# Kernel tuning notes

Hardware: AMD Instinct MI355X
Metric: run time of the kernel (lower is better)

Reference implementation:

```python
import jax, jax.numpy as jnp
import numpy as np

B, T, D, E, P = 4, 2048, 1024, 8, 1024

def setup_inputs() -> dict:
    key = jax.random.key(0)
    k1, k2, k3 = jax.random.split(key, 3)
    x = jax.random.normal(k1, (B, T, D), dtype=jnp.float32)
    gate_w = jax.random.normal(k2, (D, E), dtype=jnp.float32) * (1.0 / np.sqrt(D))
    gate_b = jnp.zeros((E,), dtype=jnp.float32)
    expert_w = jax.random.normal(k3, (E, D, P), dtype=jnp.float32) * (1.0 / np.sqrt(D))
    expert_b = jnp.zeros((E, P), dtype=jnp.float32)
    return {"x": x, "gate_w": gate_w, "gate_b": gate_b,
            "expert_w": expert_w, "expert_b": expert_b}

def reference(x, gate_w, gate_b, expert_w, expert_b):
    # gating: Dense(E) with softmax -> [B, T, E]
    gate = jax.nn.softmax(jnp.einsum('btd,de->bte', x, gate_w) + gate_b, axis=-1)
    # all experts as one batched GEMM: [B, T, E, P]
    expert_out = jnp.einsum('btd,edp->btep', x, expert_w) + expert_b
    # gate-weighted sum over experts -> [B, T, P]
    out = jnp.einsum('bte,btep->btp', gate, expert_out)
    return out
```

## Files before the change

kernel.cpp:

```cpp
#include <hip/hip_runtime.h>
#include <hip/hip_bf16.h>
#include <math.h>

#define M_TOT 8192
#define D_DIM 1024
#define E_NUM 8
#define P_DIM 1024
#define K_TOT (E_NUM * D_DIM)

typedef __attribute__((ext_vector_type(8))) short short8;
typedef __attribute__((ext_vector_type(4))) float f32x4;
typedef __attribute__((ext_vector_type(8))) unsigned short u16x8;

static __device__ __forceinline__ unsigned short f2bf(float f) {
  unsigned u = __builtin_bit_cast(unsigned, f);
  unsigned r = (u + 0x7fffu + ((u >> 16) & 1u)) >> 16;
  return (unsigned short)r;
}

__global__ __launch_bounds__(256) void prep_m_kernel(const float* __restrict__ x,
                                                     const float* __restrict__ gw,
                                                     const float* __restrict__ gb,
                                                     const float* __restrict__ eb,
                                                     float* __restrict__ gate,
                                                     unsigned short* __restrict__ xb,
                                                     float* __restrict__ out) {
  __shared__ __align__(16) unsigned short lx[4][1024];
  const int wv   = threadIdx.x >> 6;
  const int lane = threadIdx.x & 63;
  const int row  = blockIdx.x * 4 + wv;
  const float* xr = x + (size_t)row * D_DIM;

  float acc[E_NUM];
#pragma unroll
  for (int e = 0; e < E_NUM; ++e) acc[e] = 0.f;
#pragma unroll
  for (int it = 0; it < 16; ++it) {
    const int d = it * 64 + lane;
    const float xv = xr[d];
    lx[wv][d] = f2bf(xv);
    const float4* g4 = reinterpret_cast<const float4*>(gw + (size_t)d * E_NUM);
    const float4 a = g4[0], b = g4[1];
    acc[0] += xv * a.x; acc[1] += xv * a.y; acc[2] += xv * a.z; acc[3] += xv * a.w;
    acc[4] += xv * b.x; acc[5] += xv * b.y; acc[6] += xv * b.z; acc[7] += xv * b.w;
  }
#pragma unroll
  for (int off = 32; off >= 1; off >>= 1) {
#pragma unroll
    for (int e = 0; e < E_NUM; ++e) acc[e] += __shfl_xor(acc[e], off, 64);
  }
  __syncthreads();

  float g[E_NUM], mx = -1e30f;
#pragma unroll
  for (int e = 0; e < E_NUM; ++e) { g[e] = acc[e] + gb[e]; mx = fmaxf(mx, g[e]); }
  float s = 0.f;
#pragma unroll
  for (int e = 0; e < E_NUM; ++e) { g[e] = expf(g[e] - mx); s += g[e]; }
  const float inv = 1.f / s;
#pragma unroll
  for (int e = 0; e < E_NUM; ++e) g[e] *= inv;
  if (lane == 0) {
#pragma unroll
    for (int e = 0; e < E_NUM; ++e) gate[(size_t)row * E_NUM + e] = g[e];
  }

  unsigned short* xrow = xb + (size_t)row * D_DIM;
#pragma unroll
  for (int h = 0; h < 2; ++h) {
    const int jd = lane * 2 + h;
    const int cbase = (jd >> 3) * 8 + ((jd & 7) ^ (row & 7));
    const u16x8 vv = *reinterpret_cast<const u16x8*>(&lx[wv][jd * 8]);
    *reinterpret_cast<u16x8*>(&xrow[cbase * 8]) = vv;
  }

  float* orow = out + (size_t)row * P_DIM;
#pragma unroll
  for (int q = 0; q < 4; ++q) {
    const int p = q * 256 + lane * 4;
    float4 sv = {0.f, 0.f, 0.f, 0.f};
#pragma unroll
    for (int e = 0; e < E_NUM; ++e) {
      const float4 b4 = *reinterpret_cast<const float4*>(&eb[(size_t)e * P_DIM + p]);
      sv.x += g[e] * b4.x; sv.y += g[e] * b4.y; sv.z += g[e] * b4.z; sv.w += g[e] * b4.w;
    }
    *reinterpret_cast<float4*>(&orow[p]) = sv;
  }
}

__global__ __launch_bounds__(256) void wtrans2_kernel(const float* __restrict__ w,
                                                      unsigned short* __restrict__ wt) {
  __shared__ float tile[64][65];
  const int e  = blockIdx.z;
  const int p0 = blockIdx.y * 64;
  const int d0 = blockIdx.x * 64;
  const int tx = threadIdx.x & 63;
  const int ty = threadIdx.x >> 6;
  const float* src = w + ((size_t)e * D_DIM + d0) * P_DIM + p0;
#pragma unroll
  for (int i = 0; i < 16; ++i) {
    const int dr = i * 4 + ty;
    tile[dr][tx] = src[(size_t)dr * P_DIM + tx];
  }
  __syncthreads();
#pragma unroll
  for (int i = 0; i < 16; ++i) {
    const int pr = i * 4 + ty;
    const int c = tx ^ ((pr & 7) << 3);
    wt[(size_t)(p0 + pr) * K_TOT + e * D_DIM + d0 + c] = f2bf(tile[tx][pr]);
  }
}

__global__ __launch_bounds__(256, 3) void gemm_ex2_kernel(
    const unsigned short* __restrict__ xb,
    const unsigned short* __restrict__ wt,
    const float* __restrict__ gate,
    float* __restrict__ out) {
  __shared__ unsigned short lA[128 * 64];
  __shared__ unsigned short lB[128 * 64];
  __shared__ float lG[128 * 8];

  const int tid  = threadIdx.x;
  const int lane = tid & 63;
  const int wid  = tid >> 6;
  const int wr   = wid >> 1, wc = wid & 1;

  const int bid = blockIdx.x;
  const int nt  = bid & 7;
  const int idx = bid >> 3;
  const int kh  = idx & 1;
  const int mt  = idx >> 1;
  const int m0  = mt * 128, n0 = nt * 128;

  reinterpret_cast<float4*>(lG)[tid] =
      reinterpret_cast<const float4*>(gate + (size_t)m0 * E_NUM)[tid];

  f32x4 acc[4][4];
#pragma unroll
  for (int i = 0; i < 4; ++i)
#pragma unroll
    for (int j = 0; j < 4; ++j)
#pragma unroll
      for (int k = 0; k < 4; ++k) acc[i][j][k] = 0.f;

  const int r0 = tid >> 3;
  const int c8 = tid & 7;
  const unsigned short* pAb = xb + (size_t)(m0 + r0) * D_DIM + c8 * 8;
  const unsigned short* pBb = wt + (size_t)(n0 + r0) * K_TOT + c8 * 8;

  for (int e = 0; e < 4; ++e) {
    const int eg = kh * 4 + e;
    if (e > 0) {
#pragma unroll
      for (int m = 0; m < 4; ++m) {
#pragma unroll
        for (int reg = 0; reg < 4; ++reg) {
          const int r = wr * 64 + m * 16 + (lane >> 4) * 4 + reg;
          const float ratio = lG[r * 8 + (eg - 1)] / lG[r * 8 + eg];
#pragma unroll
          for (int n = 0; n < 4; ++n) acc[m][n][reg] *= ratio;
        }
      }
    }
    const unsigned short* pB = pBb + (size_t)eg * D_DIM;
    for (int kt = 0; kt < 16; ++kt) {
      __syncthreads();
#pragma unroll
      for (int i = 0; i < 4; ++i) {
        __builtin_amdgcn_global_load_lds(
            (const __attribute__((address_space(1))) void*)(pAb + (size_t)i * 32 * D_DIM + kt * 64),
            (__attribute__((address_space(3))) void*)&lA[(tid + i * 256) * 8], 16, 0, 0);
      }
#pragma unroll
      for (int i = 0; i < 4; ++i) {
        __builtin_amdgcn_global_load_lds(
            (const __attribute__((address_space(1))) void*)(pB + (size_t)i * 32 * K_TOT + kt * 64),
            (__attribute__((address_space(3))) void*)&lB[(tid + i * 256) * 8], 16, 0, 0);
      }
      __syncthreads();
#pragma unroll
      for (int kk = 0; kk < 2; ++kk) {
        const int e0 = kk * 32 + (lane >> 4) * 8;
        short8 a[4], b[4];
#pragma unroll
        for (int m = 0; m < 4; ++m) {
          const int r = wr * 64 + m * 16 + (lane & 15);
          a[m] = *reinterpret_cast<const short8*>(&lA[r * 64 + (e0 ^ ((r & 7) << 3))]);
        }
#pragma unroll
        for (int n = 0; n < 4; ++n) {
          const int r = wc * 64 + n * 16 + (lane & 15);
          b[n] = *reinterpret_cast<const short8*>(&lB[r * 64 + (e0 ^ ((r & 7) << 3))]);
        }
#pragma unroll
        for (int m = 0; m < 4; ++m)
#pragma unroll
          for (int n = 0; n < 4; ++n)
            acc[m][n] = __builtin_amdgcn_mfma_f32_16x16x32_bf16(a[m], b[n], acc[m][n], 0, 0, 0);
      }
    }
  }

#pragma unroll
  for (int n = 0; n < 4; ++n) {
    const int cl = wc * 64 + n * 16 + (lane & 15);
#pragma unroll
    for (int m = 0; m < 4; ++m) {
#pragma unroll
      for (int reg = 0; reg < 4; ++reg) {
        const int r  = wr * 64 + m * 16 + (lane >> 4) * 4 + reg;
        const float gl = lG[r * 8 + kh * 4 + 3];
        atomicAdd(&out[(size_t)(m0 + r) * P_DIM + n0 + cl], acc[m][n][reg] * gl);
      }
    }
  }
}


__global__ __launch_bounds__(256) void gate_kernel(const float* __restrict__ x,
                                                   const float* __restrict__ gw,
                                                   const float* __restrict__ gb,
                                                   float* __restrict__ gate) {
  const int row  = blockIdx.x * 4 + (threadIdx.x >> 6);
  const int lane = threadIdx.x & 63;
  const float* xr = x + (size_t)row * D_DIM;
  float acc[E_NUM];
#pragma unroll
  for (int e = 0; e < E_NUM; ++e) acc[e] = 0.f;
#pragma unroll
  for (int it = 0; it < 16; ++it) {
    const int d = it * 64 + lane;
    const float xv = xr[d];
    const float4* g4 = reinterpret_cast<const float4*>(gw + (size_t)d * E_NUM);
    float4 a = g4[0], b = g4[1];
    acc[0] += xv * a.x; acc[1] += xv * a.y; acc[2] += xv * a.z; acc[3] += xv * a.w;
    acc[4] += xv * b.x; acc[5] += xv * b.y; acc[6] += xv * b.z; acc[7] += xv * b.w;
  }
#pragma unroll
  for (int off = 32; off >= 1; off >>= 1) {
#pragma unroll
    for (int e = 0; e < E_NUM; ++e) acc[e] += __shfl_xor(acc[e], off, 64);
  }
  if (lane == 0) {
    float v[E_NUM], mx = -1e30f;
#pragma unroll
    for (int e = 0; e < E_NUM; ++e) { v[e] = acc[e] + gb[e]; mx = fmaxf(mx, v[e]); }
    float s = 0.f;
#pragma unroll
    for (int e = 0; e < E_NUM; ++e) { v[e] = expf(v[e] - mx); s += v[e]; }
    const float inv = 1.f / s;
#pragma unroll
    for (int e = 0; e < E_NUM; ++e) gate[(size_t)row * E_NUM + e] = v[e] * inv;
  }
}

__global__ __launch_bounds__(256) void wtrans_kernel(const float* __restrict__ w,
                                                     unsigned short* __restrict__ wt) {
  __shared__ float tile[64][65];
  const int e  = blockIdx.z;
  const int p0 = blockIdx.y * 64;
  const int d0 = blockIdx.x * 64;
  const int tx = threadIdx.x & 63;
  const int ty = threadIdx.x >> 6;
  const float* src = w + ((size_t)e * D_DIM + d0) * P_DIM + p0;
#pragma unroll
  for (int i = 0; i < 16; ++i) {
    const int dr = i * 4 + ty;
    tile[dr][tx] = src[(size_t)dr * P_DIM + tx];
  }
  __syncthreads();
  unsigned short* dst = wt + ((size_t)e * P_DIM + p0) * D_DIM + d0;
#pragma unroll
  for (int i = 0; i < 16; ++i) {
    const int pr = i * 4 + ty;
    const int cc = tx ^ ((pr & 7) << 3);
    dst[(size_t)pr * D_DIM + cc] = f2bf(tile[tx][pr]);
  }
}

__global__ __launch_bounds__(256, 2) void moe_gemm_kernel(
    const float* __restrict__ x,
    const unsigned short* __restrict__ wt,
    const float* __restrict__ gate,
    const float* __restrict__ eb,
    float* __restrict__ out) {
  __shared__ unsigned short lA[128 * 64];
  __shared__ unsigned short lB[128 * 64];
  __shared__ float lG[128 * 8];
  __shared__ float lBias[E_NUM * 128];

  const int tid  = threadIdx.x;
  const int lane = tid & 63;
  const int wid  = tid >> 6;
  const int wr   = wid >> 1, wc = wid & 1;
  const int m0   = blockIdx.x * 128;
  const int n0   = blockIdx.y * 128;

  reinterpret_cast<float4*>(lG)[tid] =
      reinterpret_cast<const float4*>(gate + (size_t)m0 * E_NUM)[tid];
  {
    const int e = tid >> 5, cc = (tid & 31) * 4;
    *reinterpret_cast<float4*>(&lBias[e * 128 + cc]) =
        *reinterpret_cast<const float4*>(&eb[(size_t)e * P_DIM + n0 + cc]);
  }
  __syncthreads();

  const int rA   = tid >> 1;
  const int colA = (tid & 1) * 32;
  const float* xrow = x + (size_t)(m0 + rA) * D_DIM + colA;

  f32x4 acc[4][4];
#pragma unroll
  for (int i = 0; i < 4; ++i)
#pragma unroll
    for (int jj = 0; jj < 4; ++jj)
#pragma unroll
      for (int k = 0; k < 4; ++k) acc[i][jj][k] = 0.f;

  for (int e = 0; e < E_NUM; ++e) {
    const float gs = lG[rA * 8 + e];
    const unsigned short* wte = wt + ((size_t)e * P_DIM + n0) * D_DIM;
    for (int kt = 0; kt < 16; ++kt) {
      __syncthreads();
      const float4* apv = reinterpret_cast<const float4*>(xrow + kt * 64);
#pragma unroll
      for (int jj = 0; jj < 4; ++jj) {
        float4 p = apv[2 * jj], q = apv[2 * jj + 1];
        u16x8 v;
        v[0] = f2bf(p.x * gs); v[1] = f2bf(p.y * gs);
        v[2] = f2bf(p.z * gs); v[3] = f2bf(p.w * gs);
        v[4] = f2bf(q.x * gs); v[5] = f2bf(q.y * gs);
        v[6] = f2bf(q.z * gs); v[7] = f2bf(q.w * gs);
        const int idxw = rA * 64 + ((colA + jj * 8) ^ ((rA & 7) << 3));
        *reinterpret_cast<u16x8*>(&lA[idxw]) = v;
      }
#pragma unroll
      for (int i = 0; i < 4; ++i) {
        const int u  = tid + i * 256;
        const int rr = u >> 3;
        const int cc = u & 7;
        const unsigned short* src = wte + (size_t)rr * D_DIM + kt * 64 + cc * 8;
        __builtin_amdgcn_global_load_lds(
            (const __attribute__((address_space(1))) void*)src,
            (__attribute__((address_space(3))) void*)&lB[u * 8], 16, 0, 0);
      }
      __syncthreads();
#pragma unroll
      for (int kk = 0; kk < 2; ++kk) {
        const int e0 = kk * 32 + (lane >> 4) * 8;
        short8 a[4], b[4];
#pragma unroll
        for (int m = 0; m < 4; ++m) {
          const int r = wr * 64 + m * 16 + (lane & 15);
          a[m] = *reinterpret_cast<const short8*>(&lA[r * 64 + (e0 ^ ((r & 7) << 3))]);
        }
#pragma unroll
        for (int n = 0; n < 4; ++n) {
          const int r = wc * 64 + n * 16 + (lane & 15);
          b[n] = *reinterpret_cast<const short8*>(&lB[r * 64 + (e0 ^ ((r & 7) << 3))]);
        }
#pragma unroll
        for (int m = 0; m < 4; ++m)
#pragma unroll
          for (int n = 0; n < 4; ++n)
            acc[m][n] = __builtin_amdgcn_mfma_f32_16x16x32_bf16(a[m], b[n], acc[m][n], 0, 0, 0);
      }
    }
  }

#pragma unroll
  for (int m = 0; m < 4; ++m) {
#pragma unroll
    for (int n = 0; n < 4; ++n) {
      const int rbase = wr * 64 + m * 16 + ((lane >> 4) * 4);
      const int cl    = wc * 64 + n * 16 + (lane & 15);
#pragma unroll
      for (int reg = 0; reg < 4; ++reg) {
        const int r = rbase + reg;
        float bsum = 0.f;
#pragma unroll
        for (int e = 0; e < E_NUM; ++e) bsum += lG[r * 8 + e] * lBias[e * 128 + cl];
        out[(size_t)(m0 + r) * P_DIM + n0 + cl] = acc[m][n][reg] + bsum;
      }
    }
  }
}


extern "C" void kernel_launch(void* const* d_in, const int* in_sizes, int n_in,
                              void* d_out, int out_size, void* d_ws, size_t ws_size,
                              hipStream_t stream) {
  const float* x  = (const float*)d_in[0];
  const float* gw = (const float*)d_in[1];
  const float* gb = (const float*)d_in[2];
  const float* ew = (const float*)d_in[3];
  const float* eb = (const float*)d_in[4];
  float* out = (float*)d_out;

  char* ws = (char*)d_ws;
  float* gate        = (float*)ws;
  unsigned short* wt = (unsigned short*)(ws + 262144);

  const size_t need_new = 262144ull + 16777216ull + 16777216ull;

  if (ws_size >= need_new) {
    unsigned short* xbb = (unsigned short*)(ws + 262144 + 16777216);
    wtrans2_kernel<<<dim3(D_DIM / 64, P_DIM / 64, E_NUM), 256, 0, stream>>>(ew, wt);
    prep_m_kernel<<<M_TOT / 4, 256, 0, stream>>>(x, gw, gb, eb, gate, xbb, out);
    gemm_ex2_kernel<<<1024, 256, 0, stream>>>(xbb, wt, gate, out);
  } else {
    gate_kernel<<<M_TOT / 4, 256, 0, stream>>>(x, gw, gb, gate);
    wtrans_kernel<<<dim3(D_DIM / 64, P_DIM / 64, E_NUM), 256, 0, stream>>>(ew, wt);
    moe_gemm_kernel<<<dim3(M_TOT / 128, P_DIM / 128), 256, 0, stream>>>(x, wt, gate, eb, out);
  }
}
```

Before: 193.2 us.

## Fuse weight transpose and activation prep into one launch with vectorized stores

Merges the expert-weight transpose/bf16 conversion kernel and the gating/activation-prep kernel into a single launch, with block index ranges selecting which job a block does. This removes one kernel launch and lets the two independent prep phases run at the same time on the GPU. The transpose path now packs eight bf16 values per thread into one 16-byte store instead of scalar 2-byte stores, keeping the same swizzled layout at 8-element-chunk granularity. The combined kernel allocates both shared-memory arrays in every block, which may lower occupancy.

```diff
diff --git a/kernel.cpp b/kernel.cpp
--- a/kernel.cpp
+++ b/kernel.cpp
@@ -18,96 +18,104 @@
   return (unsigned short)r;
 }
 
-__global__ __launch_bounds__(256) void prep_m_kernel(const float* __restrict__ x,
-                                                     const float* __restrict__ gw,
-                                                     const float* __restrict__ gb,
-                                                     const float* __restrict__ eb,
-                                                     float* __restrict__ gate,
-                                                     unsigned short* __restrict__ xb,
-                                                     float* __restrict__ out) {
+__global__ __launch_bounds__(256) void prep_all_kernel(const float* __restrict__ x,
+                                                       const float* __restrict__ gw,
+                                                       const float* __restrict__ gb,
+                                                       const float* __restrict__ ew,
+                                                       const float* __restrict__ eb,
+                                                       float* __restrict__ gate,
+                                                       unsigned short* __restrict__ xb,
+                                                       unsigned short* __restrict__ wt,
+                                                       float* __restrict__ out) {
   __shared__ __align__(16) unsigned short lx[4][1024];
-  const int wv   = threadIdx.x >> 6;
-  const int lane = threadIdx.x & 63;
-  const int row  = blockIdx.x * 4 + wv;
-  const float* xr = x + (size_t)row * D_DIM;
-
-  float acc[E_NUM];
-#pragma unroll
-  for (int e = 0; e < E_NUM; ++e) acc[e] = 0.f;
-#pragma unroll
-  for (int it = 0; it < 16; ++it) {
-    const int d = it * 64 + lane;
-    const float xv = xr[d];
-    lx[wv][d] = f2bf(xv);
-    const float4* g4 = reinterpret_cast<const float4*>(gw + (size_t)d * E_NUM);
-    const float4 a = g4[0], b = g4[1];
-    acc[0] += xv * a.x; acc[1] += xv * a.y; acc[2] += xv * a.z; acc[3] += xv * a.w;
-    acc[4] += xv * b.x; acc[5] += xv * b.y; acc[6] += xv * b.z; acc[7] += xv * b.w;
-  }
-#pragma unroll
-  for (int off = 32; off >= 1; off >>= 1) {
-#pragma unroll
-    for (int e = 0; e < E_NUM; ++e) acc[e] += __shfl_xor(acc[e], off, 64);
-  }
-  __syncthreads();
-
-  float g[E_NUM], mx = -1e30f;
-#pragma unroll
-  for (int e = 0; e < E_NUM; ++e) { g[e] = acc[e] + gb[e]; mx = fmaxf(mx, g[e]); }
-  float s = 0.f;
-#pragma unroll
-  for (int e = 0; e < E_NUM; ++e) { g[e] = expf(g[e] - mx); s += g[e]; }
-  const float inv = 1.f / s;
-#pragma unroll
-  for (int e = 0; e < E_NUM; ++e) g[e] *= inv;
-  if (lane == 0) {
-#pragma unroll
-    for (int e = 0; e < E_NUM; ++e) gate[(size_t)row * E_NUM + e] = g[e];
-  }
-
-  unsigned short* xrow = xb + (size_t)row * D_DIM;
-#pragma unroll
-  for (int h = 0; h < 2; ++h) {
-    const int jd = lane * 2 + h;
-    const int cbase = (jd >> 3) * 8 + ((jd & 7) ^ (row & 7));
-    const u16x8 vv = *reinterpret_cast<const u16x8*>(&lx[wv][jd * 8]);
-    *reinterpret_cast<u16x8*>(&xrow[cbase * 8]) = vv;
-  }
-
-  float* orow = out + (size_t)row * P_DIM;
-#pragma unroll
-  for (int q = 0; q < 4; ++q) {
-    const int p = q * 256 + lane * 4;
-    float4 sv = {0.f, 0.f, 0.f, 0.f};
-#pragma unroll
-    for (int e = 0; e < E_NUM; ++e) {
-      const float4 b4 = *reinterpret_cast<const float4*>(&eb[(size_t)e * P_DIM + p]);
-      sv.x += g[e] * b4.x; sv.y += g[e] * b4.y; sv.z += g[e] * b4.z; sv.w += g[e] * b4.w;
-    }
-    *reinterpret_cast<float4*>(&orow[p]) = sv;
-  }
-}
-
-__global__ __launch_bounds__(256) void wtrans2_kernel(const float* __restrict__ w,
-                                                      unsigned short* __restrict__ wt) {
   __shared__ float tile[64][65];
-  const int e  = blockIdx.z;
-  const int p0 = blockIdx.y * 64;
-  const int d0 = blockIdx.x * 64;
-  const int tx = threadIdx.x & 63;
-  const int ty = threadIdx.x >> 6;
-  const float* src = w + ((size_t)e * D_DIM + d0) * P_DIM + p0;
-#pragma unroll
-  for (int i = 0; i < 16; ++i) {
-    const int dr = i * 4 + ty;
-    tile[dr][tx] = src[(size_t)dr * P_DIM + tx];
-  }
-  __syncthreads();
-#pragma unroll
-  for (int i = 0; i < 16; ++i) {
-    const int pr = i * 4 + ty;
-    const int c = tx ^ ((pr & 7) << 3);
-    wt[(size_t)(p0 + pr) * K_TOT + e * D_DIM + d0 + c] = f2bf(tile[tx][pr]);
+
+  if (blockIdx.x < 2048) {
+    const int wv   = threadIdx.x >> 6;
+    const int lane = threadIdx.x & 63;
+    const int row  = blockIdx.x * 4 + wv;
+    const float* xr = x + (size_t)row * D_DIM;
+
+    float acc[E_NUM];
+#pragma unroll
+    for (int e = 0; e < E_NUM; ++e) acc[e] = 0.f;
+#pragma unroll
+    for (int it = 0; it < 16; ++it) {
+      const int d = it * 64 + lane;
+      const float xv = xr[d];
+      lx[wv][d] = f2bf(xv);
+      const float4* g4 = reinterpret_cast<const float4*>(gw + (size_t)d * E_NUM);
+      const float4 a = g4[0], b = g4[1];
+      acc[0] += xv * a.x; acc[1] += xv * a.y; acc[2] += xv * a.z; acc[3] += xv * a.w;
+      acc[4] += xv * b.x; acc[5] += xv * b.y; acc[6] += xv * b.z; acc[7] += xv * b.w;
+    }
+#pragma unroll
+    for (int off = 32; off >= 1; off >>= 1) {
+#pragma unroll
+      for (int e = 0; e < E_NUM; ++e) acc[e] += __shfl_xor(acc[e], off, 64);
+    }
+    __syncthreads();
+
+    float g[E_NUM], mx = -1e30f;
+#pragma unroll
+    for (int e = 0; e < E_NUM; ++e) { g[e] = acc[e] + gb[e]; mx = fmaxf(mx, g[e]); }
+    float s = 0.f;
+#pragma unroll
+    for (int e = 0; e < E_NUM; ++e) { g[e] = expf(g[e] - mx); s += g[e]; }
+    const float inv = 1.f / s;
+#pragma unroll
+    for (int e = 0; e < E_NUM; ++e) g[e] *= inv;
+    if (lane == 0) {
+#pragma unroll
+      for (int e = 0; e < E_NUM; ++e) gate[(size_t)row * E_NUM + e] = g[e];
+    }
+
+    unsigned short* xrow = xb + (size_t)row * D_DIM;
+#pragma unroll
+    for (int h = 0; h < 2; ++h) {
+      const int jd = lane * 2 + h;
+      const int cbase = (jd >> 3) * 8 + ((jd & 7) ^ (row & 7));
+      const u16x8 vv = *reinterpret_cast<const u16x8*>(&lx[wv][jd * 8]);
+      *reinterpret_cast<u16x8*>(&xrow[cbase * 8]) = vv;
+    }
+
+    float* orow = out + (size_t)row * P_DIM;
+#pragma unroll
+    for (int q = 0; q < 4; ++q) {
+      const int p = q * 256 + lane * 4;
+      float4 sv = {0.f, 0.f, 0.f, 0.f};
+#pragma unroll
+      for (int e = 0; e < E_NUM; ++e) {
+        const float4 b4 = *reinterpret_cast<const float4*>(&eb[(size_t)e * P_DIM + p]);
+        sv.x += g[e] * b4.x; sv.y += g[e] * b4.y; sv.z += g[e] * b4.z; sv.w += g[e] * b4.w;
+      }
+      *reinterpret_cast<float4*>(&orow[p]) = sv;
+    }
+  } else {
+    const int bid2 = blockIdx.x - 2048;
+    const int e  = bid2 >> 8;
+    const int p0 = ((bid2 >> 4) & 15) * 64;
+    const int d0 = (bid2 & 15) * 64;
+    const int tx = threadIdx.x & 63;
+    const int ty = threadIdx.x >> 6;
+    const float* src = ew + ((size_t)e * D_DIM + d0) * P_DIM + p0;
+#pragma unroll
+    for (int i = 0; i < 16; ++i) {
+      const int dr = i * 4 + ty;
+      tile[dr][tx] = src[(size_t)dr * P_DIM + tx];
+    }
+    __syncthreads();
+#pragma unroll
+    for (int h = 0; h < 2; ++h) {
+      const int u  = threadIdx.x + h * 256;
+      const int pr = u >> 3;
+      const int ch = u & 7;
+      u16x8 v;
+#pragma unroll
+      for (int j = 0; j < 8; ++j) v[j] = f2bf(tile[ch * 8 + j][pr]);
+      const int cs = ch ^ (pr & 7);
+      *reinterpret_cast<u16x8*>(&wt[(size_t)(p0 + pr) * K_TOT + e * D_DIM + d0 + cs * 8]) = v;
+    }
   }
 }
 
@@ -405,8 +413,7 @@
 
   if (ws_size >= need_new) {
     unsigned short* xbb = (unsigned short*)(ws + 262144 + 16777216);
-    wtrans2_kernel<<<dim3(D_DIM / 64, P_DIM / 64, E_NUM), 256, 0, stream>>>(ew, wt);
-    prep_m_kernel<<<M_TOT / 4, 256, 0, stream>>>(x, gw, gb, eb, gate, xbb, out);
+    prep_all_kernel<<<4096, 256, 0, stream>>>(x, gw, gb, ew, eb, gate, xbb, wt, out);
     gemm_ex2_kernel<<<1024, 256, 0, stream>>>(xbb, wt, gate, out);
   } else {
     gate_kernel<<<M_TOT / 4, 256, 0, stream>>>(x, gw, gb, gate);
```

New measurement: 188.9 us, median of 2. 1.02x faster.
